# Optimization experiments

Hardware: AMD Instinct MI355X
Metric: run time of the kernel (lower is better)

## Reference

```python
import jax, jax.numpy as jnp
import numpy as np

N = 100000   # nodes
E = 1600000  # edges (avg degree 16)
DIM = 128    # feature dim
EPS = 1e-6
NEG_SLOPE = 0.2  # tf.nn.leaky_relu default alpha


def layernorm(x, g, b):
    m = jnp.mean(x, axis=-1, keepdims=True)
    v = jnp.mean(jnp.square(x - m), axis=-1, keepdims=True)
    return g * (x - m) * jax.lax.rsqrt(v + EPS) + b


def setup_inputs() -> dict:
    key = jax.random.key(0)
    ks = jax.random.split(key, 12)
    s = 1.0 / np.sqrt(DIM)
    return {
        "query": jax.random.normal(ks[0], (N, DIM), jnp.float32),
        "adj_val": jax.random.uniform(ks[1], (E,), jnp.float32),
        "w_W": jax.random.normal(ks[2], (DIM, DIM), jnp.float32) * s,
        "w_b": jnp.zeros((DIM,), jnp.float32),
        "w1_W": jax.random.normal(ks[3], (DIM, DIM), jnp.float32) * s,
        "w1_b": jnp.zeros((DIM,), jnp.float32),
        "w2_W": jax.random.normal(ks[4], (DIM, DIM), jnp.float32) * s,
        "w2_b": jnp.zeros((DIM,), jnp.float32),
        "ln1_g": jnp.ones((DIM,), jnp.float32),
        "ln1_b": jnp.zeros((DIM,), jnp.float32),
        "ln2_g": jnp.ones((DIM,), jnp.float32),
        "ln2_b": jnp.zeros((DIM,), jnp.float32),
        "adj_row": jnp.sort(jax.random.randint(ks[5], (E,), 0, N, jnp.int32)),
        "adj_col": jax.random.randint(ks[6], (E,), 0, N, jnp.int32),
    }


def reference(query, adj_val, w_W, w_b, w1_W, w1_b, w2_W, w2_b,
              ln1_g, ln1_b, ln2_g, ln2_b, adj_row, adj_col):
    q = layernorm(query, ln1_g, ln1_b)          # [N, D]
    k = q                                        # key is None -> key = query
    value = k @ w_W + w_b                        # [N, D]

    # per-node scalar scores (mean_sum=False branch); dropout in eval mode (identity)
    sum1 = jnp.tanh(jnp.sum(q @ w1_W + w1_b, axis=1))   # [N]
    sum2 = jnp.tanh(jnp.sum(k @ w2_W + w2_b, axis=1))   # [N]

    # sparse add of col-scaled and row-scaled adjacency, then leaky_relu
    logits = jax.nn.leaky_relu(
        adj_val * sum1[adj_row] + adj_val * sum2[adj_col], NEG_SLOPE)  # [E]

    # sparse row-wise softmax over nonzeros
    row_max = jax.ops.segment_max(logits, adj_row, num_segments=N)
    ex = jnp.exp(logits - row_max[adj_row])
    row_sum = jax.ops.segment_sum(ex, adj_row, num_segments=N)
    attn = ex / row_sum[adj_row]                 # [E]

    # spmm: out[i] = sum_e attn[e] * value[col[e]]
    out = jax.ops.segment_sum(attn[:, None] * value[adj_col], adj_row,
                              num_segments=N)    # [N, D]
    return layernorm(out, ln2_g, ln2_b)
```

## Files before the change

kernel.cpp:

```cpp
#include <hip/hip_runtime.h>
#include <hip/hip_bf16.h>

typedef __attribute__((ext_vector_type(8))) short short8;
typedef __attribute__((ext_vector_type(8))) unsigned short ushort8;
typedef __attribute__((ext_vector_type(4))) float f32x4;
typedef __attribute__((ext_vector_type(4))) unsigned int uint4v;

#define DIM 128
#define EPS 1e-6f

__device__ __forceinline__ float wave_sum(float v){
  #pragma unroll
  for (int m = 32; m >= 1; m >>= 1) v += __shfl_xor(v, m);
  return v;
}

__global__ void setup_kernel(const float* __restrict__ w_W,
                             const float* __restrict__ w1_W, const float* __restrict__ w1_b,
                             const float* __restrict__ w2_W, const float* __restrict__ w2_b,
                             const int* __restrict__ adj_row,
                             __hip_bfloat16* __restrict__ wt_bf,
                             float* __restrict__ u1, float* __restrict__ u2,
                             float* __restrict__ c12,
                             int* __restrict__ row_ptr, int N, int E){
  const int b = blockIdx.x, tid = threadIdx.x;
  if (b == 0){
    if (tid < DIM){
      float s1 = 0.f, s2 = 0.f;
      for (int j = 0; j < DIM; ++j){ s1 += w1_W[tid*DIM + j]; s2 += w2_W[tid*DIM + j]; }
      u1[tid] = s1; u2[tid] = s2;
    }
    if (tid < 64){
      float c1 = w1_b[tid] + w1_b[tid + 64];
      float c2 = w2_b[tid] + w2_b[tid + 64];
      c1 = wave_sum(c1); c2 = wave_sum(c2);
      if (tid == 0){ c12[0] = c1; c12[1] = c2; }
    }
  } else if (b <= 64){
    int idx = (b - 1) * 256 + tid;
    int j = idx >> 7, d = idx & 127;
    wt_bf[idx] = __float2bfloat16(w_W[d*DIM + j]);
  } else {
    int r = (b - 65) * 256 + tid;
    if (r <= N){
      int lo = 0, hi = E;
      while (lo < hi){ int mid = (lo + hi) >> 1; if (adj_row[mid] < r) lo = mid + 1; else hi = mid; }
      row_ptr[r] = lo;
    }
  }
}

__launch_bounds__(256)
__global__ void node_kernel(const float* __restrict__ query,
                            const __hip_bfloat16* __restrict__ wt_bf,
                            const float* __restrict__ w_b,
                            const float* __restrict__ ln1_g, const float* __restrict__ ln1_b,
                            const float* __restrict__ u1, const float* __restrict__ u2,
                            const float* __restrict__ c12,
                            unsigned char* __restrict__ value_q,
                            float* __restrict__ s_val,
                            float* __restrict__ sum1, float* __restrict__ sum2, int N){
  __shared__ __hip_bfloat16 A[64][136];
  const int tid  = threadIdx.x;
  const int lane = tid & 63;
  const int w    = tid >> 6;
  const int q16  = lane >> 4;
  const int lq   = lane & 15;
  const int base = blockIdx.x * 64;

  float uu1[8], uu2[8], gg[8], bv[8];
  {
    const float* p1 = u1 + lq*8; const float* p2 = u2 + lq*8;
    const float* pg = ln1_g + lq*8; const float* pb = ln1_b + lq*8;
    #pragma unroll
    for (int j = 0; j < 8; ++j){ uu1[j]=p1[j]; uu2[j]=p2[j]; gg[j]=pg[j]; bv[j]=pb[j]; }
  }
  const float c1 = c12[0], c2 = c12[1];

  #pragma unroll
  for (int it = 0; it < 4; ++it){
    const int row = w*16 + it*4 + q16;
    const int n   = base + row;
    float x[8];
    if (n < N){
      const float* qp = query + (size_t)n*DIM + lq*8;
      #pragma unroll
      for (int j = 0; j < 8; ++j) x[j] = qp[j];
    } else {
      #pragma unroll
      for (int j = 0; j < 8; ++j) x[j] = 0.f;
    }
    float s = 0.f, s2 = 0.f;
    #pragma unroll
    for (int j = 0; j < 8; ++j){ s += x[j]; s2 += x[j]*x[j]; }
    #pragma unroll
    for (int m = 1; m <= 8; m <<= 1){ s += __shfl_xor(s, m); s2 += __shfl_xor(s2, m); }
    const float mean = s * (1.f/128.f);
    const float var  = s2 * (1.f/128.f) - mean*mean;
    const float rs   = rsqrtf(var + EPS);

    float p1 = 0.f, p2 = 0.f;
    unsigned pk[4];
    #pragma unroll
    for (int j = 0; j < 4; ++j){
      float n0 = gg[2*j]   * (x[2*j]   - mean) * rs + bv[2*j];
      float n1 = gg[2*j+1] * (x[2*j+1] - mean) * rs + bv[2*j+1];
      p1 += n0*uu1[2*j] + n1*uu1[2*j+1];
      p2 += n0*uu2[2*j] + n1*uu2[2*j+1];
      union { __hip_bfloat16 h; unsigned short u; } a_, b_;
      a_.h = __float2bfloat16(n0); b_.h = __float2bfloat16(n1);
      pk[j] = ((unsigned)b_.u << 16) | (unsigned)a_.u;
    }
    uint4v pv = { pk[0], pk[1], pk[2], pk[3] };
    *(uint4v*)&A[row][lq*8] = pv;
    #pragma unroll
    for (int m = 1; m <= 8; m <<= 1){ p1 += __shfl_xor(p1, m); p2 += __shfl_xor(p2, m); }
    if (lq == 0 && n < N){
      sum1[n] = tanhf(p1 + c1);
      sum2[n] = tanhf(p2 + c2);
    }
  }
  __syncthreads();

  const int rh = (w & 1) * 32;
  const int ch = (w >> 1) * 64;
  short8 afr[2][4];
  #pragma unroll
  for (int m = 0; m < 2; ++m)
    #pragma unroll
    for (int ks = 0; ks < 4; ++ks)
      afr[m][ks] = *(const short8*)&A[rh + m*16 + lq][ks*32 + q16*8];
  __syncthreads();

  #pragma unroll
  for (int jj = 0; jj < 4; ++jj){
    const int colb = ch + jj*16;
    f32x4 acc[2];
    acc[0] = (f32x4){0.f,0.f,0.f,0.f};
    acc[1] = (f32x4){0.f,0.f,0.f,0.f};
    #pragma unroll
    for (int ks = 0; ks < 4; ++ks){
      short8 bfr = *(const short8*)(wt_bf + (size_t)(colb + lq)*DIM + ks*32 + q16*8);
      acc[0] = __builtin_amdgcn_mfma_f32_16x16x32_bf16(afr[0][ks], bfr, acc[0], 0, 0, 0);
      acc[1] = __builtin_amdgcn_mfma_f32_16x16x32_bf16(afr[1][ks], bfr, acc[1], 0, 0, 0);
    }
    const int col  = colb + lq;
    const float bias = w_b[col];
    #pragma unroll
    for (int m = 0; m < 2; ++m)
      #pragma unroll
      for (int i = 0; i < 4; ++i)
        A[rh + m*16 + q16*4 + i][col] = __float2bfloat16(acc[m][i] + bias);
  }
  __syncthreads();

  const int row = tid >> 2, seg = tid & 3;
  const int n = base + row;
  float vals[32];
  float amax = 0.f;
  #pragma unroll
  for (int j = 0; j < 32; ++j){
    vals[j] = __bfloat162float(A[row][seg*32 + j]);
    amax = fmaxf(amax, fabsf(vals[j]));
  }
  amax = fmaxf(amax, __shfl_xor(amax, 1));
  amax = fmaxf(amax, __shfl_xor(amax, 2));
  const float qs = amax > 0.f ? 127.f / amax : 0.f;
  if (n < N){
    if (seg == 0) s_val[n] = amax * (1.f/127.f);
    unsigned dw[8];
    #pragma unroll
    for (int d = 0; d < 8; ++d){
      unsigned q0 = (unsigned)__float2int_rn(fmaf(vals[4*d+0], qs, 128.f));
      unsigned q1 = (unsigned)__float2int_rn(fmaf(vals[4*d+1], qs, 128.f));
      unsigned q2 = (unsigned)__float2int_rn(fmaf(vals[4*d+2], qs, 128.f));
      unsigned q3 = (unsigned)__float2int_rn(fmaf(vals[4*d+3], qs, 128.f));
      dw[d] = q0 | (q1 << 8) | (q2 << 16) | (q3 << 24);
    }
    uint4v* dst = (uint4v*)(value_q + (size_t)n*DIM + seg*32);
    dst[0] = (uint4v){dw[0], dw[1], dw[2], dw[3]};
    dst[1] = (uint4v){dw[4], dw[5], dw[6], dw[7]};
  }
}

__global__ void pack_kernel(const float* __restrict__ adj_val, const int* __restrict__ adj_row,
                            const int* __restrict__ adj_col,
                            const float* __restrict__ sum1, const float* __restrict__ sum2,
                            const float* __restrict__ s_val,
                            float2* __restrict__ excol, int E){
  int e = blockIdx.x * 256 + threadIdx.x;
  if (e >= E) return;
  float av = adj_val[e];
  int r = adj_row[e], c = adj_col[e];
  float x = av * (sum1[r] + sum2[c]);
  float lg = x > 0.f ? x : 0.2f * x;
  excol[e] = make_float2(__expf(lg) * s_val[c], __int_as_float(c));
}

__launch_bounds__(256)
__global__ void edge_kernel(const float2* __restrict__ excol, const int* __restrict__ row_ptr,
                            const unsigned char* __restrict__ value_q,
                            const float* __restrict__ ln2_g, const float* __restrict__ ln2_b,
                            float* __restrict__ out, int N){
  const int lane = threadIdx.x & 63;
  const int r = blockIdx.x * 4 + (threadIdx.x >> 6);
  if (r >= N) return;
  const int e0 = row_ptr[r], e1 = row_ptr[r+1];
  const int q  = lane >> 4;
  const int lq = lane & 15;

  float acc[8];
  #pragma unroll
  for (int j = 0; j < 8; ++j) acc[j] = 0.f;
  float sumw = 0.f;

  for (int eb = e0 + q; eb < e1; eb += 16){
    #pragma unroll
    for (int t = 0; t < 4; ++t){
      const int e = eb + t*4;
      float2 ecv = (e < e1) ? excol[e] : make_float2(0.f, __int_as_float(0));
      const float ws = ecv.x;
      const int   ck = __float_as_int(ecv.y);
      uint2 v = *(const uint2*)(value_q + ((size_t)ck << 7) + lq*8);
      sumw += ws;
      acc[0] += ws * (float)( v.x        & 0xff);
      acc[1] += ws * (float)((v.x >>  8) & 0xff);
      acc[2] += ws * (float)((v.x >> 16) & 0xff);
      acc[3] += ws * (float)( v.x >> 24);
      acc[4] += ws * (float)( v.y        & 0xff);
      acc[5] += ws * (float)((v.y >>  8) & 0xff);
      acc[6] += ws * (float)((v.y >> 16) & 0xff);
      acc[7] += ws * (float)( v.y >> 24);
    }
  }

  #pragma unroll
  for (int j = 0; j < 8; ++j){
    acc[j] += __shfl_xor(acc[j], 16);
    acc[j] += __shfl_xor(acc[j], 32);
  }
  sumw += __shfl_xor(sumw, 16);
  sumw += __shfl_xor(sumw, 32);

  const float bias = 128.f * sumw;
  #pragma unroll
  for (int j = 0; j < 8; ++j) acc[j] -= bias;

  float sx = 0.f, sxx = 0.f;
  #pragma unroll
  for (int j = 0; j < 8; ++j){ sx += acc[j]; sxx += acc[j]*acc[j]; }
  #pragma unroll
  for (int m = 1; m <= 8; m <<= 1){ sx += __shfl_xor(sx, m); sxx += __shfl_xor(sxx, m); }
  const float mean = sx * (1.f/128.f);
  const float var  = sxx * (1.f/128.f) - mean*mean;
  const float rs   = rsqrtf(var + EPS);

  if (q == 0){
    float4 g0 = ((const float4*)ln2_g)[lq*2], g1 = ((const float4*)ln2_g)[lq*2+1];
    float4 b0 = ((const float4*)ln2_b)[lq*2], b1 = ((const float4*)ln2_b)[lq*2+1];
    float4 o0, o1;
    o0.x = g0.x*(acc[0]-mean)*rs + b0.x; o0.y = g0.y*(acc[1]-mean)*rs + b0.y;
    o0.z = g0.z*(acc[2]-mean)*rs + b0.z; o0.w = g0.w*(acc[3]-mean)*rs + b0.w;
    o1.x = g1.x*(acc[4]-mean)*rs + b1.x; o1.y = g1.y*(acc[5]-mean)*rs + b1.y;
    o1.z = g1.z*(acc[6]-mean)*rs + b1.z; o1.w = g1.w*(acc[7]-mean)*rs + b1.w;
    float4* op = (float4*)(out + (size_t)r*DIM + lq*8);
    op[0] = o0; op[1] = o1;
  }
}

extern "C" void kernel_launch(void* const* d_in, const int* in_sizes, int n_in,
                              void* d_out, int out_size, void* d_ws, size_t ws_size,
                              hipStream_t stream){
  const float* query   = (const float*)d_in[0];
  const float* adj_val = (const float*)d_in[1];
  const float* w_W     = (const float*)d_in[2];
  const float* w_b     = (const float*)d_in[3];
  const float* w1_W    = (const float*)d_in[4];
  const float* w1_b    = (const float*)d_in[5];
  const float* w2_W    = (const float*)d_in[6];
  const float* w2_b    = (const float*)d_in[7];
  const float* ln1_g   = (const float*)d_in[8];
  const float* ln1_b   = (const float*)d_in[9];
  const float* ln2_g   = (const float*)d_in[10];
  const float* ln2_b   = (const float*)d_in[11];
  const int*   adj_row = (const int*)d_in[12];
  const int*   adj_col = (const int*)d_in[13];

  const int N = in_sizes[0] / DIM;
  const int E = in_sizes[1];

  char* ws = (char*)d_ws;
  size_t off = 0;
  unsigned char* value_q = (unsigned char*)(ws + off); off += (size_t)N * DIM;
  float* s_val  = (float*)(ws + off); off += (size_t)N * 4;
  float* sum1   = (float*)(ws + off); off += (size_t)N * 4;
  float* sum2   = (float*)(ws + off); off += (size_t)N * 4;
  int* row_ptr  = (int*)(ws + off);   off += (size_t)(N + 2) * 4;
  float* u1     = (float*)(ws + off); off += DIM * 4;
  float* u2     = (float*)(ws + off); off += DIM * 4;
  float* c12    = (float*)(ws + off); off += 2 * 4;
  off = (off + 63) & ~(size_t)63;
  __hip_bfloat16* wt_bf = (__hip_bfloat16*)(ws + off); off += DIM * DIM * 2;
  off = (off + 63) & ~(size_t)63;
  float2* excol = (float2*)(ws + off);

  const int rp_blocks = (N + 1 + 255) / 256;
  setup_kernel<<<65 + rp_blocks, 256, 0, stream>>>(w_W, w1_W, w1_b, w2_W, w2_b, adj_row,
                                                   wt_bf, u1, u2, c12, row_ptr, N, E);
  node_kernel<<<(N + 63) / 64, 256, 0, stream>>>(query, wt_bf, w_b, ln1_g, ln1_b,
                                                 u1, u2, c12, value_q, s_val,
                                                 sum1, sum2, N);
  pack_kernel<<<(E + 255) / 256, 256, 0, stream>>>(adj_val, adj_row, adj_col,
                                                   sum1, sum2, s_val, excol, E);
  edge_kernel<<<(N + 3) / 4, 256, 0, stream>>>(excol, row_ptr, value_q,
                                               ln2_g, ln2_b, (float*)d_out, N);
}
```

Before: 114.6 us.

## Fuse row_ptr build into pack kernel, pack sum2/scale, pre-shift column offsets

The row_ptr construction moves from per-row binary searches in the setup kernel to boundary detection inside the per-edge pack kernel. sum2 and the per-node quantization scale are interleaved into one float2 array, so pack does a single gather per column instead of two. Column indices are stored pre-shifted by 7 so the edge kernel skips the shift. The edge kernel accumulates in packed float2 vectors, and the LDS reads use vectorized ushort8 loads. Together these aim to cut gather traffic and instruction count, at the cost of serial row_ptr fill loops on threads that hit row boundaries and a 32-bit limit on the pre-shifted offset.

```diff
diff --git a/kernel.cpp b/kernel.cpp
--- a/kernel.cpp
+++ b/kernel.cpp
@@ -4,6 +4,7 @@
 typedef __attribute__((ext_vector_type(8))) short short8;
 typedef __attribute__((ext_vector_type(8))) unsigned short ushort8;
 typedef __attribute__((ext_vector_type(4))) float f32x4;
+typedef __attribute__((ext_vector_type(2))) float f32x2;
 typedef __attribute__((ext_vector_type(4))) unsigned int uint4v;
 
 #define DIM 128
@@ -18,11 +19,9 @@
 __global__ void setup_kernel(const float* __restrict__ w_W,
                              const float* __restrict__ w1_W, const float* __restrict__ w1_b,
                              const float* __restrict__ w2_W, const float* __restrict__ w2_b,
-                             const int* __restrict__ adj_row,
                              __hip_bfloat16* __restrict__ wt_bf,
                              float* __restrict__ u1, float* __restrict__ u2,
-                             float* __restrict__ c12,
-                             int* __restrict__ row_ptr, int N, int E){
+                             float* __restrict__ c12){
   const int b = blockIdx.x, tid = threadIdx.x;
   if (b == 0){
     if (tid < DIM){
@@ -36,17 +35,10 @@
       c1 = wave_sum(c1); c2 = wave_sum(c2);
       if (tid == 0){ c12[0] = c1; c12[1] = c2; }
     }
-  } else if (b <= 64){
+  } else {
     int idx = (b - 1) * 256 + tid;
     int j = idx >> 7, d = idx & 127;
     wt_bf[idx] = __float2bfloat16(w_W[d*DIM + j]);
-  } else {
-    int r = (b - 65) * 256 + tid;
-    if (r <= N){
-      int lo = 0, hi = E;
-      while (lo < hi){ int mid = (lo + hi) >> 1; if (adj_row[mid] < r) lo = mid + 1; else hi = mid; }
-      row_ptr[r] = lo;
-    }
   }
 }
 
@@ -58,8 +50,7 @@
                             const float* __restrict__ u1, const float* __restrict__ u2,
                             const float* __restrict__ c12,
                             unsigned char* __restrict__ value_q,
-                            float* __restrict__ s_val,
-                            float* __restrict__ sum1, float* __restrict__ sum2, int N){
+                            float* __restrict__ sum1, float2* __restrict__ s2v, int N){
   __shared__ __hip_bfloat16 A[64][136];
   const int tid  = threadIdx.x;
   const int lane = tid & 63;
@@ -116,8 +107,8 @@
     #pragma unroll
     for (int m = 1; m <= 8; m <<= 1){ p1 += __shfl_xor(p1, m); p2 += __shfl_xor(p2, m); }
     if (lq == 0 && n < N){
-      sum1[n] = tanhf(p1 + c1);
-      sum2[n] = tanhf(p2 + c2);
+      sum1[n]   = tanhf(p1 + c1);
+      s2v[n].x  = tanhf(p2 + c2);
     }
   }
   __syncthreads();
@@ -158,16 +149,22 @@
   const int n = base + row;
   float vals[32];
   float amax = 0.f;
-  #pragma unroll
-  for (int j = 0; j < 32; ++j){
-    vals[j] = __bfloat162float(A[row][seg*32 + j]);
-    amax = fmaxf(amax, fabsf(vals[j]));
+  const ushort8* ap = (const ushort8*)&A[row][seg*32];
+  #pragma unroll
+  for (int h = 0; h < 4; ++h){
+    ushort8 vv = ap[h];
+    #pragma unroll
+    for (int j = 0; j < 8; ++j){
+      float f = __uint_as_float((unsigned)vv[j] << 16);
+      vals[h*8 + j] = f;
+      amax = fmaxf(amax, fabsf(f));
+    }
   }
   amax = fmaxf(amax, __shfl_xor(amax, 1));
   amax = fmaxf(amax, __shfl_xor(amax, 2));
   const float qs = amax > 0.f ? 127.f / amax : 0.f;
   if (n < N){
-    if (seg == 0) s_val[n] = amax * (1.f/127.f);
+    if (seg == 0) s2v[n].y = amax * (1.f/127.f);
     unsigned dw[8];
     #pragma unroll
     for (int d = 0; d < 8; ++d){
@@ -185,16 +182,25 @@
 
 __global__ void pack_kernel(const float* __restrict__ adj_val, const int* __restrict__ adj_row,
                             const int* __restrict__ adj_col,
-                            const float* __restrict__ sum1, const float* __restrict__ sum2,
-                            const float* __restrict__ s_val,
-                            float2* __restrict__ excol, int E){
+                            const float* __restrict__ sum1, const float2* __restrict__ s2v,
+                            float2* __restrict__ excol, int* __restrict__ row_ptr,
+                            int N, int E){
   int e = blockIdx.x * 256 + threadIdx.x;
   if (e >= E) return;
+  int r  = adj_row[e];
+  int rp = (e > 0) ? adj_row[e-1] : -1;
+  if (rp != r){
+    for (int rr = rp + 1; rr <= r; ++rr) row_ptr[rr] = e;
+  }
+  if (e == E - 1){
+    for (int rr = r + 1; rr <= N; ++rr) row_ptr[rr] = E;
+  }
   float av = adj_val[e];
-  int r = adj_row[e], c = adj_col[e];
-  float x = av * (sum1[r] + sum2[c]);
+  int c = adj_col[e];
+  float2 sv = s2v[c];
+  float x = av * (sum1[r] + sv.x);
   float lg = x > 0.f ? x : 0.2f * x;
-  excol[e] = make_float2(__expf(lg) * s_val[c], __int_as_float(c));
+  excol[e] = make_float2(__expf(lg) * sv.y, __int_as_float(c << 7));
 }
 
 __launch_bounds__(256)
@@ -208,10 +214,11 @@
   const int e0 = row_ptr[r], e1 = row_ptr[r+1];
   const int q  = lane >> 4;
   const int lq = lane & 15;
-
-  float acc[8];
-  #pragma unroll
-  for (int j = 0; j < 8; ++j) acc[j] = 0.f;
+  const unsigned char* vbase = value_q + lq*8;
+
+  f32x2 acc2[4];
+  #pragma unroll
+  for (int j = 0; j < 4; ++j) acc2[j] = (f32x2){0.f, 0.f};
   float sumw = 0.f;
 
   for (int eb = e0 + q; eb < e1; eb += 16){
@@ -219,36 +226,40 @@
     for (int t = 0; t < 4; ++t){
       const int e = eb + t*4;
       float2 ecv = (e < e1) ? excol[e] : make_float2(0.f, __int_as_float(0));
-      const float ws = ecv.x;
-      const int   ck = __float_as_int(ecv.y);
-      uint2 v = *(const uint2*)(value_q + ((size_t)ck << 7) + lq*8);
-      sumw += ws;
-      acc[0] += ws * (float)( v.x        & 0xff);
-      acc[1] += ws * (float)((v.x >>  8) & 0xff);
-      acc[2] += ws * (float)((v.x >> 16) & 0xff);
-      acc[3] += ws * (float)( v.x >> 24);
-      acc[4] += ws * (float)( v.y        & 0xff);
-      acc[5] += ws * (float)((v.y >>  8) & 0xff);
-      acc[6] += ws * (float)((v.y >> 16) & 0xff);
-      acc[7] += ws * (float)( v.y >> 24);
-    }
-  }
-
-  #pragma unroll
-  for (int j = 0; j < 8; ++j){
-    acc[j] += __shfl_xor(acc[j], 16);
-    acc[j] += __shfl_xor(acc[j], 32);
+      const float wsc = ecv.x;
+      const unsigned voff = (unsigned)__float_as_int(ecv.y);
+      uint2 v = *(const uint2*)(vbase + voff);
+      sumw += wsc;
+      f32x2 w2 = { wsc, wsc };
+      f32x2 p0 = { (float)( v.x        & 0xff), (float)((v.x >>  8) & 0xff) };
+      f32x2 p1 = { (float)((v.x >> 16) & 0xff), (float)( v.x >> 24)         };
+      f32x2 p2 = { (float)( v.y        & 0xff), (float)((v.y >>  8) & 0xff) };
+      f32x2 p3 = { (float)((v.y >> 16) & 0xff), (float)( v.y >> 24)         };
+      acc2[0] += w2 * p0;
+      acc2[1] += w2 * p1;
+      acc2[2] += w2 * p2;
+      acc2[3] += w2 * p3;
+    }
+  }
+
+  #pragma unroll
+  for (int j = 0; j < 4; ++j){
+    acc2[j].x += __shfl_xor(acc2[j].x, 16); acc2[j].y += __shfl_xor(acc2[j].y, 16);
+    acc2[j].x += __shfl_xor(acc2[j].x, 32); acc2[j].y += __shfl_xor(acc2[j].y, 32);
   }
   sumw += __shfl_xor(sumw, 16);
   sumw += __shfl_xor(sumw, 32);
 
   const float bias = 128.f * sumw;
   #pragma unroll
-  for (int j = 0; j < 8; ++j) acc[j] -= bias;
+  for (int j = 0; j < 4; ++j){ acc2[j].x -= bias; acc2[j].y -= bias; }
 
   float sx = 0.f, sxx = 0.f;
   #pragma unroll
-  for (int j = 0; j < 8; ++j){ sx += acc[j]; sxx += acc[j]*acc[j]; }
+  for (int j = 0; j < 4; ++j){
+    sx  += acc2[j].x + acc2[j].y;
+    sxx += acc2[j].x*acc2[j].x + acc2[j].y*acc2[j].y;
+  }
   #pragma unroll
   for (int m = 1; m <= 8; m <<= 1){ sx += __shfl_xor(sx, m); sxx += __shfl_xor(sxx, m); }
   const float mean = sx * (1.f/128.f);
@@ -259,10 +270,10 @@
     float4 g0 = ((const float4*)ln2_g)[lq*2], g1 = ((const float4*)ln2_g)[lq*2+1];
     float4 b0 = ((const float4*)ln2_b)[lq*2], b1 = ((const float4*)ln2_b)[lq*2+1];
     float4 o0, o1;
-    o0.x = g0.x*(acc[0]-mean)*rs + b0.x; o0.y = g0.y*(acc[1]-mean)*rs + b0.y;
-    o0.z = g0.z*(acc[2]-mean)*rs + b0.z; o0.w = g0.w*(acc[3]-mean)*rs + b0.w;
-    o1.x = g1.x*(acc[4]-mean)*rs + b1.x; o1.y = g1.y*(acc[5]-mean)*rs + b1.y;
-    o1.z = g1.z*(acc[6]-mean)*rs + b1.z; o1.w = g1.w*(acc[7]-mean)*rs + b1.w;
+    o0.x = g0.x*(acc2[0].x-mean)*rs + b0.x; o0.y = g0.y*(acc2[0].y-mean)*rs + b0.y;
+    o0.z = g0.z*(acc2[1].x-mean)*rs + b0.z; o0.w = g0.w*(acc2[1].y-mean)*rs + b0.w;
+    o1.x = g1.x*(acc2[2].x-mean)*rs + b1.x; o1.y = g1.y*(acc2[2].y-mean)*rs + b1.y;
+    o1.z = g1.z*(acc2[3].x-mean)*rs + b1.z; o1.w = g1.w*(acc2[3].y-mean)*rs + b1.w;
     float4* op = (float4*)(out + (size_t)r*DIM + lq*8);
     op[0] = o0; op[1] = o1;
   }
@@ -292,9 +303,8 @@
   char* ws = (char*)d_ws;
   size_t off = 0;
   unsigned char* value_q = (unsigned char*)(ws + off); off += (size_t)N * DIM;
-  float* s_val  = (float*)(ws + off); off += (size_t)N * 4;
   float* sum1   = (float*)(ws + off); off += (size_t)N * 4;
-  float* sum2   = (float*)(ws + off); off += (size_t)N * 4;
+  float2* s2v   = (float2*)(ws + off); off += (size_t)N * 8;
   int* row_ptr  = (int*)(ws + off);   off += (size_t)(N + 2) * 4;
   float* u1     = (float*)(ws + off); off += DIM * 4;
   float* u2     = (float*)(ws + off); off += DIM * 4;
@@ -304,14 +314,11 @@
   off = (off + 63) & ~(size_t)63;
   float2* excol = (float2*)(ws + off);
 
-  const int rp_blocks = (N + 1 + 255) / 256;
-  setup_kernel<<<65 + rp_blocks, 256, 0, stream>>>(w_W, w1_W, w1_b, w2_W, w2_b, adj_row,
-                                                   wt_bf, u1, u2, c12, row_ptr, N, E);
+  setup_kernel<<<65, 256, 0, stream>>>(w_W, w1_W, w1_b, w2_W, w2_b, wt_bf, u1, u2, c12);
   node_kernel<<<(N + 63) / 64, 256, 0, stream>>>(query, wt_bf, w_b, ln1_g, ln1_b,
-                                                 u1, u2, c12, value_q, s_val,
-                                                 sum1, sum2, N);
+                                                 u1, u2, c12, value_q, sum1, s2v, N);
   pack_kernel<<<(E + 255) / 256, 256, 0, stream>>>(adj_val, adj_row, adj_col,
-                                                   sum1, sum2, s_val, excol, E);
+                                                   sum1, s2v, excol, row_ptr, N, E);
   edge_kernel<<<(N + 3) / 4, 256, 0, stream>>>(excol, row_ptr, value_q,
                                                ln2_g, ln2_b, (float*)d_out, N);
 }
```

New measurement: 106.4 us. 7.2% less time.
